# Kernel tuning notes

Hardware: AMD Instinct MI355X
Metric: run time of the kernel (lower is better)

Reference implementation:

```python
import jax, jax.numpy as jnp
import numpy as np

B, T, D, H = 4, 2048, 1024, 16
HD = D // H  # 64


def setup_inputs() -> dict:
    key = jax.random.key(0)
    ks = jax.random.split(key, 5)
    return {
        "x": jax.random.normal(ks[0], (B, T, D), dtype=jnp.float32),
        "W_qkv": jax.random.normal(ks[1], (D, 3 * D), dtype=jnp.float32) * 0.02,
        "b_qkv": jax.random.normal(ks[2], (3 * D,), dtype=jnp.float32) * 0.02,
        "W_out": jax.random.normal(ks[3], (D, D), dtype=jnp.float32) * 0.02,
        "b_out": jax.random.normal(ks[4], (D,), dtype=jnp.float32) * 0.02,
        "mask": 1,
    }


def reference(x, W_qkv, b_qkv, W_out, b_out, mask):
    # fused QKV projection: (B,T,3D)
    qkv = x @ W_qkv + b_qkv
    # torch layout: view (B,T,H,3*hd) then chunk last dim into q,k,v
    qkv = qkv.reshape(B, T, H, 3, HD)
    q = qkv[..., 0, :].transpose(0, 2, 1, 3)  # (B,H,T,hd)
    k = qkv[..., 1, :].transpose(0, 2, 1, 3)
    v = qkv[..., 2, :].transpose(0, 2, 1, 3)
    scores = jnp.einsum('bhqd,bhkd->bhqk', q, k) / jnp.sqrt(jnp.float32(HD))
    if mask:
        causal = jnp.triu(jnp.ones((T, T), dtype=bool), k=1)
        scores = jnp.where(causal[None, None], jnp.float32(-jnp.inf), scores)
    attn = jax.nn.softmax(scores, axis=-1)
    out = jnp.einsum('bhqk,bhkd->bhqd', attn, v)  # (B,H,T,hd)
    out = out.transpose(0, 2, 1, 3).reshape(B, T, D)
    return out @ W_out + b_out
```

## Files before the change

kernel.cpp:

```cpp
#include <hip/hip_runtime.h>

typedef unsigned short u16;
typedef __bf16 bf16x8 __attribute__((ext_vector_type(8)));
typedef float f32x4 __attribute__((ext_vector_type(4)));
typedef float f32x16 __attribute__((ext_vector_type(16)));

#define DEV __device__ __forceinline__

constexpr int Bb = 4, Tt = 2048, Dd = 1024, Hh = 16, HDd = 64;
constexpr int MM = Bb * Tt;
constexpr float QSCALE = 0.125f * 1.4426950408889634f;

DEV u16 f2bf(float f) {
  unsigned u = __float_as_uint(f);
  u += 0x7fffu + ((u >> 16) & 1u);
  return (u16)(u >> 16);
}

DEV unsigned cvtpk(float a, float b) {
  unsigned r;
  asm("v_cvt_pk_bf16_f32 %0, %1, %2" : "=v"(r) : "v"(a), "v"(b));
  return r;
}

DEV void pswap(unsigned& a, unsigned& b) {
  asm("v_permlane32_swap_b32 %0, %1" : "+v"(a), "+v"(b));
}

DEV void gload_lds16(const u16* g, u16* l) {
  __builtin_amdgcn_global_load_lds(
      (const __attribute__((address_space(1))) void*)g,
      (__attribute__((address_space(3))) void*)l, 16, 0, 0);
}

__global__ __launch_bounds__(256) void cast_x_kernel(const float* __restrict__ in,
                                                     u16* __restrict__ out, int n8) {
  int i = blockIdx.x * 256 + threadIdx.x;
  if (i >= n8) return;
  const float4* p = (const float4*)in + (size_t)i * 2;
  float4 v0 = p[0], v1 = p[1];
  union { u16 u[8]; uint4 v; } t;
  t.u[0] = f2bf(v0.x); t.u[1] = f2bf(v0.y); t.u[2] = f2bf(v0.z); t.u[3] = f2bf(v0.w);
  t.u[4] = f2bf(v1.x); t.u[5] = f2bf(v1.y); t.u[6] = f2bf(v1.z); t.u[7] = f2bf(v1.w);
  ((uint4*)out)[i] = t.v;
}

__global__ __launch_bounds__(256) void wcast_t_kernel(const float* __restrict__ in,
                                                      u16* __restrict__ out, int K, int N) {
  __shared__ float tile[32][33];
  int n0 = blockIdx.x * 32, k0 = blockIdx.y * 32;
  int tx = threadIdx.x & 31, ty = threadIdx.x >> 5;
  #pragma unroll
  for (int yy = ty; yy < 32; yy += 8)
    tile[yy][tx] = in[(size_t)(k0 + yy) * N + n0 + tx];
  __syncthreads();
  #pragma unroll
  for (int yy = ty; yy < 32; yy += 8)
    out[(size_t)(n0 + yy) * K + k0 + tx] = f2bf(tile[tx][yy]);
}

__global__ __launch_bounds__(256) void vtrans_kernel(const u16* __restrict__ V,
                                                     u16* __restrict__ Vt) {
  __shared__ u16 tile[32][33];
  size_t base = (size_t)blockIdx.z * Tt * HDd;
  int t0 = blockIdx.x * 32, d0 = blockIdx.y * 32;
  int tx = threadIdx.x & 31, ty = threadIdx.x >> 5;
  #pragma unroll
  for (int yy = ty; yy < 32; yy += 8)
    tile[yy][tx] = V[base + (size_t)(t0 + yy) * HDd + d0 + tx];
  __syncthreads();
  #pragma unroll
  for (int yy = ty; yy < 32; yy += 8)
    Vt[base + (size_t)(d0 + yy) * Tt + t0 + tx] = tile[tx][yy];
}

DEV void stage_tile(const u16* __restrict__ src, int row0, int k0, int ld, u16* lds) {
  int t = threadIdx.x, w = t >> 6;
  #pragma unroll
  for (int j = 0; j < 2; ++j) {
    int e = (j * 256 + t) * 8;
    int r = e >> 5;
    int slot = (e >> 3) & 3;
    int c = (slot ^ ((r >> 1) & 3)) << 3;
    gload_lds16(src + (size_t)(row0 + r) * ld + k0 + c, lds + j * 2048 + w * 512);
  }
}

template <int EPI>
__global__ __launch_bounds__(256) void gemm_bt_kernel(
    const u16* __restrict__ A, const u16* __restrict__ Bt,
    const float* __restrict__ bias, float* __restrict__ Cf,
    u16* __restrict__ Qb, u16* __restrict__ Kb, u16* __restrict__ Vb,
    int M, int N, int Kd) {
  __shared__ __align__(16) u16 SH[16384];
  int nx = N >> 7;
  int bid = blockIdx.y * nx + blockIdx.x;
  int nwg = (M >> 7) * nx;
  int swz = (bid & 7) * (nwg >> 3) + (bid >> 3);
  int m0 = (swz / nx) * 128, n0 = (swz % nx) * 128;

  int tid = threadIdx.x, l = tid & 63, w = tid >> 6;
  int lo = l & 15, g = l >> 4;
  int wm = (w >> 1) * 64, wn = (w & 1) * 64;
  f32x4 acc[4][4] = {};
  stage_tile(A, m0, 0, Kd, SH);
  stage_tile(Bt, n0, 0, Kd, SH + 8192);
  __syncthreads();
  int nk = Kd >> 5;
  for (int kt = 0; kt < nk; ++kt) {
    int cur = kt & 1;
    if (kt + 1 < nk) {
      stage_tile(A, m0, (kt + 1) * 32, Kd, SH + (cur ^ 1) * 4096);
      stage_tile(Bt, n0, (kt + 1) * 32, Kd, SH + 8192 + (cur ^ 1) * 4096);
    }
    const u16* Ac = SH + cur * 4096;
    const u16* Bc = SH + 8192 + cur * 4096;
    bf16x8 a[4], b[4];
    #pragma unroll
    for (int i = 0; i < 4; ++i) {
      int row = wm + i * 16 + lo;
      a[i] = *(const bf16x8*)&Ac[row * 32 + ((g ^ ((row >> 1) & 3)) << 3)];
    }
    #pragma unroll
    for (int j = 0; j < 4; ++j) {
      int row = wn + j * 16 + lo;
      b[j] = *(const bf16x8*)&Bc[row * 32 + ((g ^ ((row >> 1) & 3)) << 3)];
    }
    #pragma unroll
    for (int i = 0; i < 4; ++i)
      #pragma unroll
      for (int j = 0; j < 4; ++j)
        acc[i][j] = __builtin_amdgcn_mfma_f32_16x16x32_bf16(a[i], b[j], acc[i][j], 0, 0, 0);
    __syncthreads();
  }
  if (EPI == 0) {
    u16* ep = SH + w * 4096;
    int nblk = n0 + wn;
    int hh = nblk / 192, which = (nblk % 192) >> 6;
    float qs = (which == 0) ? QSCALE : 1.0f;
    #pragma unroll
    for (int j = 0; j < 4; ++j) {
      float bv = bias[nblk + j * 16 + lo];
      int slot = j * 2 + (lo >> 3);
      #pragma unroll
      for (int i = 0; i < 4; ++i) {
        #pragma unroll
        for (int r = 0; r < 4; ++r) {
          int lrow = i * 16 + g * 4 + r;
          ep[lrow * 64 + ((slot ^ (lrow & 7)) << 3) + (lo & 7)] =
              f2bf((acc[i][j][r] + bv) * qs);
        }
      }
    }
    asm volatile("s_waitcnt lgkmcnt(0)" ::: "memory");
    u16* dst = (which == 0) ? Qb : (which == 1) ? Kb : Vb;
    int mblk = m0 + wm;
    int b_ = mblk >> 11, t0 = mblk & (Tt - 1);
    dst += ((size_t)(b_ * Hh + hh) * Tt + t0) * HDd;
    #pragma unroll
    for (int s = 0; s < 8; ++s) {
      int row = s * 8 + (l >> 3);
      int phys = ((l & 7) ^ (row & 7)) << 3;
      uint4 v = *(const uint4*)&ep[row * 64 + phys];
      *(uint4*)(dst + row * 64 + (l & 7) * 8) = v;
    }
  } else {
    #pragma unroll
    for (int j = 0; j < 4; ++j) {
      int n = n0 + wn + j * 16 + lo;
      float bv = bias[n];
      #pragma unroll
      for (int i = 0; i < 4; ++i) {
        #pragma unroll
        for (int r = 0; r < 4; ++r) {
          int m = m0 + wm + i * 16 + g * 4 + r;
          Cf[(size_t)m * N + n] = acc[i][j][r] + bv;
        }
      }
    }
  }
}

DEV void stage64x64(const u16* __restrict__ g, size_t rstride, u16* lds) {
  int t = threadIdx.x, w = t >> 6;
  #pragma unroll
  for (int j = 0; j < 2; ++j) {
    int e = j * 256 + t;
    int r = e >> 3, p = e & 7;
    int lg = p ^ (r & 7);
    gload_lds16(g + (size_t)r * rstride + lg * 8, lds + (size_t)(j * 256 + w * 64) * 8);
  }
}

DEV void build_pfrags(const f32x16& s, bf16x8& f0, bf16x8& f1) {
  unsigned w0 = cvtpk(s[0], s[1]),  w1 = cvtpk(s[2], s[3]);
  unsigned w2 = cvtpk(s[4], s[5]),  w3 = cvtpk(s[6], s[7]);
  unsigned w4 = cvtpk(s[8], s[9]),  w5 = cvtpk(s[10], s[11]);
  unsigned w6 = cvtpk(s[12], s[13]), w7 = cvtpk(s[14], s[15]);
  pswap(w0, w2);
  pswap(w1, w3);
  pswap(w4, w6);
  pswap(w5, w7);
  union { unsigned u[4]; bf16x8 v; } t0, t1;
  t0.u[0] = w0; t0.u[1] = w1; t0.u[2] = w2; t0.u[3] = w3;
  t1.u[0] = w4; t1.u[1] = w5; t1.u[2] = w6; t1.u[3] = w7;
  f0 = t0.v; f1 = t1.v;
}

DEV void write_o(u16* __restrict__ O, size_t rowbase, const f32x16& o0,
                 const f32x16& o1, float L, int hf) {
  float inv = 1.0f / L;
  #pragma unroll
  for (int m = 0; m < 4; ++m) {
    uint2 v0, v1;
    v0.x = cvtpk(o0[4 * m] * inv,     o0[4 * m + 1] * inv);
    v0.y = cvtpk(o0[4 * m + 2] * inv, o0[4 * m + 3] * inv);
    *(uint2*)(O + rowbase + m * 8 + hf * 4) = v0;
    v1.x = cvtpk(o1[4 * m] * inv,     o1[4 * m + 1] * inv);
    v1.y = cvtpk(o1[4 * m + 2] * inv, o1[4 * m + 3] * inv);
    *(uint2*)(O + rowbase + 32 + m * 8 + hf * 4) = v1;
  }
}

__global__ __launch_bounds__(256) void attn_kernel(const u16* __restrict__ Q,
                                                   const u16* __restrict__ K,
                                                   const u16* __restrict__ Vt,
                                                   u16* __restrict__ O) {
  __shared__ __align__(16) u16 Ks[2][4096];
  __shared__ __align__(16) u16 Vs[2][4096];
  int bh = blockIdx.y;
  int b_ = bh >> 4, h = bh & 15;
  const u16* Qp = Q + (size_t)bh * Tt * HDd;
  const u16* Kp = K + (size_t)bh * Tt * HDd;
  const u16* Vp = Vt + (size_t)bh * HDd * Tt;
  int tid = threadIdx.x, w = tid >> 6, l = tid & 63;
  int lq = l & 31, hf = l >> 5;
  int p = blockIdx.x;
  int JA = 15 - p, JB = p;
  int ntA = 2 * JA + 2, ntB = 2 * JB + 2, ntT = ntA + ntB;

  int q0 = 128 * JA + 32 * w;
  int qrow = q0 + lq;

  bf16x8 aq[4];
  #pragma unroll
  for (int s = 0; s < 4; ++s)
    aq[s] = *(const bf16x8*)(Qp + (size_t)qrow * HDd + s * 16 + hf * 8);

  f32x16 o0 = {}, o1 = {};
  float M = -1e30f, L = 0.f;

  stage64x64(Kp, HDd, Ks[0]);
  stage64x64(Vp, Tt, Vs[0]);
  __syncthreads();

  for (int it = 0; it < ntT; ++it) {
    if (it == ntA) {
      size_t rbA = ((size_t)b_ * Tt + qrow) * Dd + h * HDd;
      write_o(O, rbA, o0, o1, L, hf);
      #pragma unroll
      for (int r = 0; r < 16; ++r) { o0[r] = 0.f; o1[r] = 0.f; }
      M = -1e30f; L = 0.f;
      q0 = 128 * JB + 32 * w;
      qrow = q0 + lq;
      #pragma unroll
      for (int s = 0; s < 4; ++s)
        aq[s] = *(const bf16x8*)(Qp + (size_t)qrow * HDd + s * 16 + hf * 8);
    }
    int kt = (it < ntA ? it : it - ntA) * 64;
    int cur = it & 1;
    if (it + 1 < ntT) {
      int nkt = (it + 1 < ntA ? it + 1 : it + 1 - ntA) * 64;
      stage64x64(Kp + (size_t)nkt * HDd, HDd, Ks[cur ^ 1]);
      stage64x64(Vp + nkt, Tt, Vs[cur ^ 1]);
    }
    if (kt < q0 + 32) {
      f32x16 s0 = {}, s1 = {};
      int swz = lq & 7;
      __builtin_amdgcn_s_setprio(1);
      #pragma unroll
      for (int ds = 0; ds < 4; ++ds) {
        int slot = 2 * ds + hf;
        bf16x8 k0 = *(const bf16x8*)&Ks[cur][lq * 64 + ((slot ^ swz) << 3)];
        bf16x8 k1 = *(const bf16x8*)&Ks[cur][(32 + lq) * 64 + ((slot ^ swz) << 3)];
        s0 = __builtin_amdgcn_mfma_f32_32x32x16_bf16(k0, aq[ds], s0, 0, 0, 0);
        s1 = __builtin_amdgcn_mfma_f32_32x32x16_bf16(k1, aq[ds], s1, 0, 0, 0);
      }
      __builtin_amdgcn_s_setprio(0);
      if (kt + 63 > q0) {
        #pragma unroll
        for (int r = 0; r < 16; ++r) {
          int kg = kt + (r & 3) + 8 * (r >> 2) + 4 * hf;
          if (kg > qrow)      s0[r] = -INFINITY;
          if (kg + 32 > qrow) s1[r] = -INFINITY;
        }
      }
      float mx_[16];
      #pragma unroll
      for (int r = 0; r < 16; ++r) mx_[r] = fmaxf(s0[r], s1[r]);
      #pragma unroll
      for (int st = 8; st >= 1; st >>= 1)
        #pragma unroll
        for (int r = 0; r < 16; ++r) if (r < st) mx_[r] = fmaxf(mx_[r], mx_[r + st]);
      float mx = fmaxf(mx_[0], __shfl_xor(mx_[0], 32));
      float sc = 1.f;
      if (!__all(mx <= M + 8.f)) {
        float Mn = fmaxf(M, mx);
        sc = __builtin_amdgcn_exp2f(M - Mn);
        M = Mn;
        #pragma unroll
        for (int r = 0; r < 16; ++r) { o0[r] *= sc; o1[r] *= sc; }
      }
      #pragma unroll
      for (int r = 0; r < 16; ++r) {
        s0[r] = __builtin_amdgcn_exp2f(s0[r] - M);
        s1[r] = __builtin_amdgcn_exp2f(s1[r] - M);
      }
      float ls_[16];
      #pragma unroll
      for (int r = 0; r < 16; ++r) ls_[r] = s0[r] + s1[r];
      #pragma unroll
      for (int st = 8; st >= 1; st >>= 1)
        #pragma unroll
        for (int r = 0; r < 16; ++r) if (r < st) ls_[r] += ls_[r + st];
      float ls = ls_[0] + __shfl_xor(ls_[0], 32);
      L = L * sc + ls;
      bf16x8 pf0, pf1, pf2, pf3;
      build_pfrags(s0, pf0, pf1);
      build_pfrags(s1, pf2, pf3);
      __builtin_amdgcn_s_setprio(1);
      #pragma unroll
      for (int ks = 0; ks < 4; ++ks) {
        int slot = 2 * ks + hf;
        bf16x8 v0 = *(const bf16x8*)&Vs[cur][lq * 64 + ((slot ^ swz) << 3)];
        bf16x8 v1 = *(const bf16x8*)&Vs[cur][(32 + lq) * 64 + ((slot ^ swz) << 3)];
        bf16x8 pf = (ks == 0) ? pf0 : (ks == 1) ? pf1 : (ks == 2) ? pf2 : pf3;
        o0 = __builtin_amdgcn_mfma_f32_32x32x16_bf16(v0, pf, o0, 0, 0, 0);
        o1 = __builtin_amdgcn_mfma_f32_32x32x16_bf16(v1, pf, o1, 0, 0, 0);
      }
      __builtin_amdgcn_s_setprio(0);
    }
    __syncthreads();
  }

  size_t rbB = ((size_t)b_ * Tt + qrow) * Dd + h * HDd;
  write_o(O, rbB, o0, o1, L, hf);
}

extern "C" void kernel_launch(void* const* d_in, const int* in_sizes, int n_in,
                              void* d_out, int out_size, void* d_ws, size_t ws_size,
                              hipStream_t stream) {
  const float* x    = (const float*)d_in[0];
  const float* Wqkv = (const float*)d_in[1];
  const float* bqkv = (const float*)d_in[2];
  const float* Wout = (const float*)d_in[3];
  const float* bout = (const float*)d_in[4];
  float* out = (float*)d_out;
  char* ws = (char*)d_ws;

  u16* xb    = (u16*)(ws + 0);
  u16* Wqkvt = (u16*)(ws + 16777216);
  u16* Woutt = (u16*)(ws + 23068672);
  u16* Qb    = (u16*)(ws + 25165824);
  u16* Kb    = (u16*)(ws + 41943040);
  u16* Vb    = (u16*)(ws + 58720256);
  u16* Vtb   = (u16*)(ws + 0);
  u16* Ob    = (u16*)(ws + 58720256);

  cast_x_kernel<<<4096, 256, 0, stream>>>(x, xb, (MM * Dd) / 8);
  wcast_t_kernel<<<dim3(96, 32), 256, 0, stream>>>(Wqkv, Wqkvt, Dd, 3 * Dd);
  wcast_t_kernel<<<dim3(32, 32), 256, 0, stream>>>(Wout, Woutt, Dd, Dd);
  gemm_bt_kernel<0><<<dim3(24, 64), 256, 0, stream>>>(
      xb, Wqkvt, bqkv, nullptr, Qb, Kb, Vb, MM, 3 * Dd, Dd);
  vtrans_kernel<<<dim3(Tt / 32, HDd / 32, Bb * Hh), 256, 0, stream>>>(Vb, Vtb);
  attn_kernel<<<dim3(8, Bb * Hh), 256, 0, stream>>>(Qb, Kb, Vtb, Ob);
  gemm_bt_kernel<1><<<dim3(8, 64), 256, 0, stream>>>(
      Ob, Woutt, bout, out, nullptr, nullptr, nullptr, MM, Dd, Dd);
}
```

Measured before the change: 188.7 us.

## Triple-buffer K/V tiles in attention with prefetch distance two and vmcnt waits

The attention kernel moves from double to triple buffering of K and V tiles in shared memory. It prefetches two tiles ahead and replaces __syncthreads with an explicit vmcnt wait plus s_barrier, so global loads stay in flight across iterations. The block index mapping is also remapped so that consecutive blocks handle different heads for the same pair index, changing how work is placed across CUs. The cost is more LDS (48KB), which may reduce occupancy, and the hardcoded vmcnt(4) assumes stage64x64 issues exactly a fixed number of loads per tile.

```diff
diff --git a/kernel.cpp b/kernel.cpp
--- a/kernel.cpp
+++ b/kernel.cpp
@@ -226,16 +226,16 @@
                                                    const u16* __restrict__ K,
                                                    const u16* __restrict__ Vt,
                                                    u16* __restrict__ O) {
-  __shared__ __align__(16) u16 Ks[2][4096];
-  __shared__ __align__(16) u16 Vs[2][4096];
-  int bh = blockIdx.y;
+  __shared__ __align__(16) u16 Ks[3][4096];
+  __shared__ __align__(16) u16 Vs[3][4096];
+  int p = blockIdx.y & 7;
+  int bh = ((int)blockIdx.y >> 3) * 8 + (int)blockIdx.x;
   int b_ = bh >> 4, h = bh & 15;
   const u16* Qp = Q + (size_t)bh * Tt * HDd;
   const u16* Kp = K + (size_t)bh * Tt * HDd;
   const u16* Vp = Vt + (size_t)bh * HDd * Tt;
   int tid = threadIdx.x, w = tid >> 6, l = tid & 63;
   int lq = l & 31, hf = l >> 5;
-  int p = blockIdx.x;
   int JA = 15 - p, JB = p;
   int ntA = 2 * JA + 2, ntB = 2 * JB + 2, ntT = ntA + ntB;
 
@@ -252,7 +252,10 @@
 
   stage64x64(Kp, HDd, Ks[0]);
   stage64x64(Vp, Tt, Vs[0]);
-  __syncthreads();
+  stage64x64(Kp + (size_t)64 * HDd, HDd, Ks[1]);
+  stage64x64(Vp + 64, Tt, Vs[1]);
+  asm volatile("s_waitcnt vmcnt(4)" ::: "memory");
+  __builtin_amdgcn_s_barrier();
 
   for (int it = 0; it < ntT; ++it) {
     if (it == ntA) {
@@ -267,13 +270,16 @@
       for (int s = 0; s < 4; ++s)
         aq[s] = *(const bf16x8*)(Qp + (size_t)qrow * HDd + s * 16 + hf * 8);
     }
+    if (it + 2 < ntT) {
+      int t2 = it + 2;
+      int nkt = (t2 < ntA ? t2 : t2 - ntA) * 64;
+      int bi = t2 % 3;
+      stage64x64(Kp + (size_t)nkt * HDd, HDd, Ks[bi]);
+      stage64x64(Vp + nkt, Tt, Vs[bi]);
+    }
     int kt = (it < ntA ? it : it - ntA) * 64;
-    int cur = it & 1;
-    if (it + 1 < ntT) {
-      int nkt = (it + 1 < ntA ? it + 1 : it + 1 - ntA) * 64;
-      stage64x64(Kp + (size_t)nkt * HDd, HDd, Ks[cur ^ 1]);
-      stage64x64(Vp + nkt, Tt, Vs[cur ^ 1]);
-    }
+    const u16* Kc = Ks[it % 3];
+    const u16* Vc = Vs[it % 3];
     if (kt < q0 + 32) {
       f32x16 s0 = {}, s1 = {};
       int swz = lq & 7;
@@ -281,8 +287,8 @@
       #pragma unroll
       for (int ds = 0; ds < 4; ++ds) {
         int slot = 2 * ds + hf;
-        bf16x8 k0 = *(const bf16x8*)&Ks[cur][lq * 64 + ((slot ^ swz) << 3)];
-        bf16x8 k1 = *(const bf16x8*)&Ks[cur][(32 + lq) * 64 + ((slot ^ swz) << 3)];
+        bf16x8 k0 = *(const bf16x8*)&Kc[lq * 64 + ((slot ^ swz) << 3)];
+        bf16x8 k1 = *(const bf16x8*)&Kc[(32 + lq) * 64 + ((slot ^ swz) << 3)];
         s0 = __builtin_amdgcn_mfma_f32_32x32x16_bf16(k0, aq[ds], s0, 0, 0, 0);
         s1 = __builtin_amdgcn_mfma_f32_32x32x16_bf16(k1, aq[ds], s1, 0, 0, 0);
       }
@@ -332,15 +338,20 @@
       #pragma unroll
       for (int ks = 0; ks < 4; ++ks) {
         int slot = 2 * ks + hf;
-        bf16x8 v0 = *(const bf16x8*)&Vs[cur][lq * 64 + ((slot ^ swz) << 3)];
-        bf16x8 v1 = *(const bf16x8*)&Vs[cur][(32 + lq) * 64 + ((slot ^ swz) << 3)];
+        bf16x8 v0 = *(const bf16x8*)&Vc[lq * 64 + ((slot ^ swz) << 3)];
+        bf16x8 v1 = *(const bf16x8*)&Vc[(32 + lq) * 64 + ((slot ^ swz) << 3)];
         bf16x8 pf = (ks == 0) ? pf0 : (ks == 1) ? pf1 : (ks == 2) ? pf2 : pf3;
         o0 = __builtin_amdgcn_mfma_f32_32x32x16_bf16(v0, pf, o0, 0, 0, 0);
         o1 = __builtin_amdgcn_mfma_f32_32x32x16_bf16(v1, pf, o1, 0, 0, 0);
       }
       __builtin_amdgcn_s_setprio(0);
     }
-    __syncthreads();
+    if (it + 2 < ntT) {
+      asm volatile("s_waitcnt vmcnt(4)" ::: "memory");
+    } else {
+      asm volatile("s_waitcnt vmcnt(0)" ::: "memory");
+    }
+    __builtin_amdgcn_s_barrier();
   }
 
   size_t rbB = ((size_t)b_ * Tt + qrow) * Dd + h * HDd;
@@ -373,7 +384,7 @@
   gemm_bt_kernel<0><<<dim3(24, 64), 256, 0, stream>>>(
       xb, Wqkvt, bqkv, nullptr, Qb, Kb, Vb, MM, 3 * Dd, Dd);
   vtrans_kernel<<<dim3(Tt / 32, HDd / 32, Bb * Hh), 256, 0, stream>>>(Vb, Vtb);
-  attn_kernel<<<dim3(8, Bb * Hh), 256, 0, stream>>>(Qb, Kb, Vtb, Ob);
+  attn_kernel<<<dim3(8, 64), 256, 0, stream>>>(Qb, Kb, Vtb, Ob);
   gemm_bt_kernel<1><<<dim3(8, 64), 256, 0, stream>>>(
       Ob, Woutt, bout, out, nullptr, nullptr, nullptr, MM, Dd, Dd);
 }
```

Measured after the change: 188.4 us. No clear change (-0.2%).
